# Performance work log

Measured on AMD Instinct MI355X. Metric: run time of the kernel, lower is better.

## Reference

```python
import jax, jax.numpy as jnp
import numpy as np

N_PATHS = 8
T2_EFF = 0.5 * 100.0 + 0.5 * (100 // 50)  # p_dimer*T2_dimer + p_trimer*T2_trimer = 51.0
J_FREQ = 20.0


def setup_inputs() -> dict:
    key = jax.random.key(0)
    ks = jax.random.split(key, 5)
    B, D, H, P = 2048, 1024, 1024, N_PATHS
    return {
        "x": jax.random.normal(ks[0], (B, D), dtype=jnp.float32),
        "W_input": jax.random.normal(ks[1], (D, H), dtype=jnp.float32) * 0.1,
        "W_paths": jax.random.normal(ks[2], (P, H, H), dtype=jnp.float32) * 0.1,
        "J_coupling": jax.random.normal(ks[3], (P, P), dtype=jnp.float32) * 0.01,
        "coherent_state": jax.random.normal(ks[4], (B, P, H), dtype=jnp.float32),
        "t": jnp.ones((1,), dtype=jnp.float32),  # time_since_formation buffer
    }


def reference(x, W_input, W_paths, J_coupling, coherent_state, t):
    # base activation: [B, H]
    base = x @ W_input
    # all per-path matmuls batched into one einsum: [B, P, H]
    path_act = jnp.einsum("bh,phk->bpk", base, W_paths)
    # coherence decay gate (scalar, broadcasts)
    alpha = jnp.clip(jnp.exp(-t[0] / T2_EFF), 0.0, 1.0)
    superposition = alpha * coherent_state + (1.0 - alpha) * path_act
    # interference matrix from symmetrized J-coupling
    J_sym = 0.5 * (J_coupling + J_coupling.T)
    phase = 2.0 * jnp.pi * J_FREQ * t[0] / 1000.0
    interference = jax.nn.softmax(jnp.cos(phase * J_sym), axis=1)  # [P, P]
    # double-loop mixing == small matmul over path dim
    interfered = jnp.einsum("ij,bjh->bih", interference, superposition) / N_PATHS
    interfered = interfered * alpha  # coherence_factor == alpha
    # no measurement (default path): mean over paths
    return jnp.mean(interfered, axis=1)  # [B, H]
```

## Files before the change

kernel.cpp:

```cpp
#include <hip/hip_runtime.h>
#include <cstdint>


typedef __attribute__((ext_vector_type(8))) __bf16 bf16x8;
typedef __attribute__((ext_vector_type(4))) float f32x4;
typedef unsigned short u16;

__device__ __forceinline__ u16 f32_to_bf16_rne(float f) {
  unsigned int u = __float_as_uint(f);
  u += 0x7fffu + ((u >> 16) & 1u);
  return (u16)(u >> 16);
}

__device__ __forceinline__ f32x4 nt_load4(const float* p) {
  return __builtin_nontemporal_load((const f32x4*)p);
}

__device__ __forceinline__ void wave_scalars(const float* __restrict__ J,
                                             const float* __restrict__ t,
                                             float* w_out, float* alpha_out) {
  const int lane = threadIdx.x & 63;
  float tv = t[0];
  float alpha = fminf(fmaxf(expf(-tv / 51.0f), 0.0f), 1.0f);
  float phase = 2.0f * 3.14159265358979323846f * 20.0f * tv / 1000.0f;
  int i = lane >> 3, j = lane & 7;
  float jsym = 0.5f * (J[i * 8 + j] + J[j * 8 + i]);
  float e = expf(cosf(phase * jsym));
  float rs = e;
  rs += __shfl_xor(rs, 1);
  rs += __shfl_xor(rs, 2);
  rs += __shfl_xor(rs, 4);
  float p = e / rs;
  float cs = p;
  cs += __shfl_xor(cs, 8);
  cs += __shfl_xor(cs, 16);
  cs += __shfl_xor(cs, 32);
  *w_out = alpha * (1.0f / 64.0f) * cs;
  *alpha_out = alpha;
}

__device__ __forceinline__ void convert16(const float* __restrict__ src,
                                          u16* __restrict__ dst, u16* ld,
                                          int tid) {
  f32x4 v[16];
#pragma unroll
  for (int row = 0; row < 16; row++) v[row] = nt_load4(src + row * 1024 + tid * 4);
#pragma unroll
  for (int row = 0; row < 16; row++) {
    ushort4 o;
    o.x = f32_to_bf16_rne(v[row][0]);
    o.y = f32_to_bf16_rne(v[row][1]);
    o.z = f32_to_bf16_rne(v[row][2]);
    o.w = f32_to_bf16_rne(v[row][3]);
    *(ushort4*)(ld + row * 1032 + tid * 4) = o;
  }
  __syncthreads();
#pragma unroll
  for (int s = 0; s < 8; s++) {
    int idx = s * 256 + tid;
    int lf = idx & 63, kt = idx >> 6;
    int row = lf & 15, colb = kt * 32 + ((lf >> 4) << 3);
    *(uint4*)(dst + (kt * 64 + lf) * 8) = *(const uint4*)(ld + row * 1032 + colb);
  }
}

__global__ __launch_bounds__(256, 4) void k_prep(
    const float* __restrict__ win, const float* __restrict__ wp,
    const float* __restrict__ J, const float* __restrict__ t,
    u16* __restrict__ winfrag, u16* __restrict__ wefrag) {
  __shared__ __align__(16) char smem[33024];
  const int blk = blockIdx.x;
  const int tid = threadIdx.x;
  const int lane = tid & 63;

  if (blk < 512) {
    float* lt = (float*)smem;
    float wv, alpha;
    wave_scalars(J, t, &wv, &alpha);
    float wLO[8];
#pragma unroll
    for (int p = 0; p < 8; p++)
      wLO[p] = __shfl(wv, (lane & 56) | p) * (1.0f - alpha);
    const int a0 = (blk & 31) * 32;
    const int b0 = (blk >> 5) * 64;
    f32x4 v[2][8];
#pragma unroll
    for (int s = 0; s < 2; s++) {
      const int item = s * 256 + tid;
      const int row = item >> 4, ch = item & 15;
      const float* base = wp + (size_t)(a0 + row) * 1024 + b0 + ch * 4;
#pragma unroll
      for (int j = 0; j < 8; j++) v[s][j] = nt_load4(base + (size_t)j * 1048576);
    }
#pragma unroll
    for (int s = 0; s < 2; s++) {
      const int item = s * 256 + tid;
      const int row = item >> 4, ch = item & 15;
      f32x4 acc = {0.f, 0.f, 0.f, 0.f};
#pragma unroll
      for (int j = 0; j < 8; j++) acc += wLO[j] * v[s][j];
      *(f32x4*)&lt[row * 68 + ch * 4] = acc;
    }
    __syncthreads();
    {
      const int lf = tid & 63, rtl = tid >> 6;
      const int rowh2 = rtl * 16 + (lf & 15);
      const int kh1 = (lf >> 4) << 3;
      __align__(16) u16 o[8];
#pragma unroll
      for (int i = 0; i < 8; i++)
        o[i] = f32_to_bf16_rne(lt[(kh1 + i) * 68 + rowh2]);
      const int rt = (b0 >> 4) + rtl, kt = a0 >> 5;
      *(uint4*)(wefrag + ((size_t)(rt * 32 + kt) * 64 + lf) * 8) = *(const uint4*)o;
    }
  } else {
    const int cid = blk - 512;
    convert16(win + (size_t)cid * 16384, winfrag + (size_t)cid * 16384,
              (u16*)smem, tid);
  }
}

__global__ __launch_bounds__(256, 4) void k_mid(
    const float* __restrict__ x, const u16* __restrict__ Af,
    const u16* __restrict__ Bf, u16* __restrict__ xfrag,
    u16* __restrict__ ofrag) {
  __shared__ __align__(16) char smem[33024];
  const int blk = blockIdx.x;
  const int tid = threadIdx.x;

  if (blk < 512) {
    u16* ct = (u16*)smem;
    const int wave = tid >> 6, lane = tid & 63;
    const int quad = lane >> 4, t16 = lane & 15;
    const int xcd = blk & 7, i = blk >> 3;
    const int m0 = (xcd + 8 * (i & 1)) * 64;
    const int n0 = (i >> 1) * 32;
    const u16* ap = Af + ((size_t)((m0 + wave * 16) >> 4) * 32) * 512 + lane * 8;
    const u16* bp = Bf + ((size_t)(n0 >> 4) * 32) * 512 + lane * 8;

    f32x4 acc[2] = {{0.f, 0.f, 0.f, 0.f}, {0.f, 0.f, 0.f, 0.f}};
    for (int kb = 0; kb < 32; kb += 4) {
      bf16x8 a[4], b0[4], b1[4];
#pragma unroll
      for (int u = 0; u < 4; u++) {
        a[u] = *(const bf16x8*)(ap + (kb + u) * 512);
        b0[u] = *(const bf16x8*)(bp + (kb + u) * 512);
        b1[u] = *(const bf16x8*)(bp + (32 + kb + u) * 512);
      }
#pragma unroll
      for (int u = 0; u < 4; u++) {
        acc[0] = __builtin_amdgcn_mfma_f32_16x16x32_bf16(a[u], b0[u], acc[0], 0, 0, 0);
        acc[1] = __builtin_amdgcn_mfma_f32_16x16x32_bf16(a[u], b1[u], acc[1], 0, 0, 0);
      }
    }
#pragma unroll
    for (int r = 0; r < 4; r++)
#pragma unroll
      for (int ni = 0; ni < 2; ni++)
        ct[(wave * 16 + quad * 4 + r) * 36 + ni * 16 + t16] =
            f32_to_bf16_rne(acc[ni][r]);
    __syncthreads();
    {
      int lf = tid & 63, rtl = tid >> 6;
      int rowl = rtl * 16 + (lf & 15);
      int colb = (lf >> 4) << 3;
      __align__(16) u16 o[8];
#pragma unroll
      for (int i2 = 0; i2 < 8; i2++) o[i2] = ct[rowl * 36 + colb + i2];
      *(uint4*)(ofrag +
                ((size_t)(((m0 >> 4) + rtl) * 32 + (n0 >> 5)) * 64 + lf) * 8) =
          *(const uint4*)o;
    }
  } else {
    const int cid = blk - 512;
    convert16(x + (size_t)cid * 16384, xfrag + (size_t)cid * 16384, (u16*)smem,
              tid);
  }
}

__global__ __launch_bounds__(512, 4) void k_main(
    const u16* __restrict__ Af, const u16* __restrict__ Bf,
    const float* __restrict__ coh, const float* __restrict__ J,
    const float* __restrict__ t, float* __restrict__ out) {
  __shared__ float cs_lds[64 * 68];
  const int tid = threadIdx.x;
  const int wave = tid >> 6, lane = tid & 63;
  const int xcd = blockIdx.x & 7, i = blockIdx.x >> 3;
  const int m0 = (xcd + 8 * (i >> 4)) * 64;
  const int n0 = (i & 15) * 64;
  const int quad = lane >> 4, t16 = lane & 15;
  const int wm = (wave >> 1) * 32, wn = (wave & 1) * 32;

  f32x4 acc[2][2];
  if (wave < 4) {
    const u16* ap = Af + ((size_t)((m0 + wm) >> 4) * 32) * 512 + lane * 8;
    const u16* bp = Bf + ((size_t)((n0 + wn) >> 4) * 32) * 512 + lane * 8;
#pragma unroll
    for (int mi = 0; mi < 2; mi++)
#pragma unroll
      for (int ni = 0; ni < 2; ni++) acc[mi][ni] = (f32x4){0.f, 0.f, 0.f, 0.f};
    for (int kb = 0; kb < 32; kb += 4) {
      bf16x8 a0[4], a1[4], b0[4], b1[4];
#pragma unroll
      for (int u = 0; u < 4; u++) {
        a0[u] = *(const bf16x8*)(ap + (kb + u) * 512);
        a1[u] = *(const bf16x8*)(ap + (32 + kb + u) * 512);
        b0[u] = *(const bf16x8*)(bp + (kb + u) * 512);
        b1[u] = *(const bf16x8*)(bp + (32 + kb + u) * 512);
      }
#pragma unroll
      for (int u = 0; u < 4; u++) {
        acc[0][0] = __builtin_amdgcn_mfma_f32_16x16x32_bf16(a0[u], b0[u], acc[0][0], 0, 0, 0);
        acc[0][1] = __builtin_amdgcn_mfma_f32_16x16x32_bf16(a0[u], b1[u], acc[0][1], 0, 0, 0);
        acc[1][0] = __builtin_amdgcn_mfma_f32_16x16x32_bf16(a1[u], b0[u], acc[1][0], 0, 0, 0);
        acc[1][1] = __builtin_amdgcn_mfma_f32_16x16x32_bf16(a1[u], b1[u], acc[1][1], 0, 0, 0);
      }
    }
  } else {
    float wv, alpha;
    wave_scalars(J, t, &wv, &alpha);
    float wHI[8];
#pragma unroll
    for (int p = 0; p < 8; p++) wHI[p] = __shfl(wv, (lane & 56) | p) * alpha;
    const int tc = (wave - 4) * 64 + lane;
    const int c4 = tc & 15;
    const int rb = tc >> 4;
    const float* cb = coh + (size_t)m0 * 8192 + n0 + c4 * 4;
#pragma unroll
    for (int up = 0; up < 2; up++) {
      f32x4 v[2][8];
#pragma unroll
      for (int h = 0; h < 2; h++) {
        const float* cr = cb + (size_t)(rb + 16 * (up * 2 + h)) * 8192;
#pragma unroll
        for (int p = 0; p < 8; p++) v[h][p] = nt_load4(cr + p * 1024);
      }
#pragma unroll
      for (int h = 0; h < 2; h++) {
        f32x4 a4 = {0.f, 0.f, 0.f, 0.f};
#pragma unroll
        for (int p = 0; p < 8; p++) a4 += wHI[p] * v[h][p];
        *(f32x4*)&cs_lds[(rb + 16 * (up * 2 + h)) * 68 + c4 * 4] = a4;
      }
    }
  }
  __syncthreads();
  if (wave < 4) {
#pragma unroll
    for (int mi = 0; mi < 2; mi++)
#pragma unroll
      for (int r = 0; r < 4; r++) {
        const int ml = wm + mi * 16 + quad * 4 + r;
        const size_t mrow = (size_t)(m0 + ml) * 1024;
#pragma unroll
        for (int ni = 0; ni < 2; ni++) {
          const int nl = wn + ni * 16 + t16;
          out[mrow + n0 + nl] = acc[mi][ni][r] + cs_lds[ml * 68 + nl];
        }
      }
  }
}

extern "C" void kernel_launch(void* const* d_in, const int* in_sizes, int n_in,
                              void* d_out, int out_size, void* d_ws, size_t ws_size,
                              hipStream_t stream) {
  const float* x   = (const float*)d_in[0];
  const float* win = (const float*)d_in[1];
  const float* wp  = (const float*)d_in[2];
  const float* J   = (const float*)d_in[3];
  const float* coh = (const float*)d_in[4];
  const float* t   = (const float*)d_in[5];
  float* out = (float*)d_out;

  char* ws = (char*)d_ws;
  u16* xfrag   = (u16*)ws;
  u16* winfrag = (u16*)(ws + 4u * 1024 * 1024);
  u16* wefrag  = (u16*)(ws + 6u * 1024 * 1024);
  u16* wctfrag = (u16*)(ws + 8u * 1024 * 1024);

  k_prep<<<576, 256, 0, stream>>>(win, wp, J, t, winfrag, wefrag);
  k_mid<<<640, 256, 0, stream>>>(x, wefrag, winfrag, xfrag, wctfrag);
  k_main<<<512, 512, 0, stream>>>(xfrag, wctfrag, coh, J, t, out);
}
```

Baseline: 157.1 us.

## Move x conversion into prep kernel and split main-kernel work across all waves

The x fp32-to-bf16 fragment conversion moves from the middle kernel into the prep kernel, so the middle kernel becomes a pure small GEMM. In the main kernel, all eight waves now first stream the coherent_state tile and reduce it into LDS, then all eight run the MFMA GEMM on smaller per-wave tiles. Each wave adds its accumulator into LDS, and the output is written with vectorized 16-byte stores. This replaces the earlier split where four waves did MFMA while four did the coherent-state load, at the cost of serializing the load phase before the GEMM and adding an extra barrier.

```diff
diff --git a/kernel.cpp b/kernel.cpp
--- a/kernel.cpp
+++ b/kernel.cpp
@@ -12,7 +12,7 @@
   return (u16)(u >> 16);
 }
 
-__device__ __forceinline__ f32x4 nt_load4(const float* p) {
+__device__ __forceinline__ f32x4 nt4(const float* p) {
   return __builtin_nontemporal_load((const f32x4*)p);
 }
 
@@ -44,7 +44,7 @@
                                           int tid) {
   f32x4 v[16];
 #pragma unroll
-  for (int row = 0; row < 16; row++) v[row] = nt_load4(src + row * 1024 + tid * 4);
+  for (int row = 0; row < 16; row++) v[row] = nt4(src + row * 1024 + tid * 4);
 #pragma unroll
   for (int row = 0; row < 16; row++) {
     ushort4 o;
@@ -65,8 +65,9 @@
 }
 
 __global__ __launch_bounds__(256, 4) void k_prep(
-    const float* __restrict__ win, const float* __restrict__ wp,
-    const float* __restrict__ J, const float* __restrict__ t,
+    const float* __restrict__ x, const float* __restrict__ win,
+    const float* __restrict__ wp, const float* __restrict__ J,
+    const float* __restrict__ t, u16* __restrict__ xfrag,
     u16* __restrict__ winfrag, u16* __restrict__ wefrag) {
   __shared__ __align__(16) char smem[33024];
   const int blk = blockIdx.x;
@@ -90,7 +91,7 @@
       const int row = item >> 4, ch = item & 15;
       const float* base = wp + (size_t)(a0 + row) * 1024 + b0 + ch * 4;
 #pragma unroll
-      for (int j = 0; j < 8; j++) v[s][j] = nt_load4(base + (size_t)j * 1048576);
+      for (int j = 0; j < 8; j++) v[s][j] = nt4(base + (size_t)j * 1048576);
     }
 #pragma unroll
     for (int s = 0; s < 2; s++) {
@@ -113,68 +114,62 @@
       const int rt = (b0 >> 4) + rtl, kt = a0 >> 5;
       *(uint4*)(wefrag + ((size_t)(rt * 32 + kt) * 64 + lf) * 8) = *(const uint4*)o;
     }
-  } else {
-    const int cid = blk - 512;
-    convert16(win + (size_t)cid * 16384, winfrag + (size_t)cid * 16384,
-              (u16*)smem, tid);
-  }
-}
-
-__global__ __launch_bounds__(256, 4) void k_mid(
-    const float* __restrict__ x, const u16* __restrict__ Af,
-    const u16* __restrict__ Bf, u16* __restrict__ xfrag,
-    u16* __restrict__ ofrag) {
-  __shared__ __align__(16) char smem[33024];
-  const int blk = blockIdx.x;
-  const int tid = threadIdx.x;
-
-  if (blk < 512) {
-    u16* ct = (u16*)smem;
-    const int wave = tid >> 6, lane = tid & 63;
-    const int quad = lane >> 4, t16 = lane & 15;
-    const int xcd = blk & 7, i = blk >> 3;
-    const int m0 = (xcd + 8 * (i & 1)) * 64;
-    const int n0 = (i >> 1) * 32;
-    const u16* ap = Af + ((size_t)((m0 + wave * 16) >> 4) * 32) * 512 + lane * 8;
-    const u16* bp = Bf + ((size_t)(n0 >> 4) * 32) * 512 + lane * 8;
-
-    f32x4 acc[2] = {{0.f, 0.f, 0.f, 0.f}, {0.f, 0.f, 0.f, 0.f}};
-    for (int kb = 0; kb < 32; kb += 4) {
-      bf16x8 a[4], b0[4], b1[4];
-#pragma unroll
-      for (int u = 0; u < 4; u++) {
-        a[u] = *(const bf16x8*)(ap + (kb + u) * 512);
-        b0[u] = *(const bf16x8*)(bp + (kb + u) * 512);
-        b1[u] = *(const bf16x8*)(bp + (32 + kb + u) * 512);
-      }
-#pragma unroll
-      for (int u = 0; u < 4; u++) {
-        acc[0] = __builtin_amdgcn_mfma_f32_16x16x32_bf16(a[u], b0[u], acc[0], 0, 0, 0);
-        acc[1] = __builtin_amdgcn_mfma_f32_16x16x32_bf16(a[u], b1[u], acc[1], 0, 0, 0);
-      }
-    }
-#pragma unroll
-    for (int r = 0; r < 4; r++)
-#pragma unroll
-      for (int ni = 0; ni < 2; ni++)
-        ct[(wave * 16 + quad * 4 + r) * 36 + ni * 16 + t16] =
-            f32_to_bf16_rne(acc[ni][r]);
-    __syncthreads();
-    {
-      int lf = tid & 63, rtl = tid >> 6;
-      int rowl = rtl * 16 + (lf & 15);
-      int colb = (lf >> 4) << 3;
-      __align__(16) u16 o[8];
-#pragma unroll
-      for (int i2 = 0; i2 < 8; i2++) o[i2] = ct[rowl * 36 + colb + i2];
-      *(uint4*)(ofrag +
-                ((size_t)(((m0 >> 4) + rtl) * 32 + (n0 >> 5)) * 64 + lf) * 8) =
-          *(const uint4*)o;
-    }
-  } else {
+  } else if (blk < 640) {
     const int cid = blk - 512;
     convert16(x + (size_t)cid * 16384, xfrag + (size_t)cid * 16384, (u16*)smem,
               tid);
+  } else {
+    const int cid = blk - 640;
+    convert16(win + (size_t)cid * 16384, winfrag + (size_t)cid * 16384,
+              (u16*)smem, tid);
+  }
+}
+
+__global__ __launch_bounds__(256, 4) void k_gemm0(const u16* __restrict__ Af,
+                                                  const u16* __restrict__ Bf,
+                                                  u16* __restrict__ ofrag) {
+  __shared__ u16 ct[64 * 36];
+  const int tid = threadIdx.x;
+  const int wave = tid >> 6, lane = tid & 63;
+  const int quad = lane >> 4, t16 = lane & 15;
+  const int xcd = blockIdx.x & 7, i = blockIdx.x >> 3;
+  const int m0 = (xcd + 8 * (i & 1)) * 64;
+  const int n0 = (i >> 1) * 32;
+  const u16* ap = Af + ((size_t)((m0 + wave * 16) >> 4) * 32) * 512 + lane * 8;
+  const u16* bp = Bf + ((size_t)(n0 >> 4) * 32) * 512 + lane * 8;
+
+  f32x4 acc[2] = {{0.f, 0.f, 0.f, 0.f}, {0.f, 0.f, 0.f, 0.f}};
+  for (int kb = 0; kb < 32; kb += 4) {
+    bf16x8 a[4], b0[4], b1[4];
+#pragma unroll
+    for (int u = 0; u < 4; u++) {
+      a[u] = *(const bf16x8*)(ap + (kb + u) * 512);
+      b0[u] = *(const bf16x8*)(bp + (kb + u) * 512);
+      b1[u] = *(const bf16x8*)(bp + (32 + kb + u) * 512);
+    }
+#pragma unroll
+    for (int u = 0; u < 4; u++) {
+      acc[0] = __builtin_amdgcn_mfma_f32_16x16x32_bf16(a[u], b0[u], acc[0], 0, 0, 0);
+      acc[1] = __builtin_amdgcn_mfma_f32_16x16x32_bf16(a[u], b1[u], acc[1], 0, 0, 0);
+    }
+  }
+#pragma unroll
+  for (int r = 0; r < 4; r++)
+#pragma unroll
+    for (int ni = 0; ni < 2; ni++)
+      ct[(wave * 16 + quad * 4 + r) * 36 + ni * 16 + t16] =
+          f32_to_bf16_rne(acc[ni][r]);
+  __syncthreads();
+  {
+    int lf = tid & 63, rtl = tid >> 6;
+    int rowl = rtl * 16 + (lf & 15);
+    int colb = (lf >> 4) << 3;
+    __align__(16) u16 o[8];
+#pragma unroll
+    for (int i2 = 0; i2 < 8; i2++) o[i2] = ct[rowl * 36 + colb + i2];
+    *(uint4*)(ofrag +
+              ((size_t)(((m0 >> 4) + rtl) * 32 + (n0 >> 5)) * 64 + lf) * 8) =
+        *(const uint4*)o;
   }
 }
 
@@ -182,82 +177,76 @@
     const u16* __restrict__ Af, const u16* __restrict__ Bf,
     const float* __restrict__ coh, const float* __restrict__ J,
     const float* __restrict__ t, float* __restrict__ out) {
-  __shared__ float cs_lds[64 * 68];
+  __shared__ float cs[64 * 68];
   const int tid = threadIdx.x;
   const int wave = tid >> 6, lane = tid & 63;
+  const int quad = lane >> 4, t16 = lane & 15;
   const int xcd = blockIdx.x & 7, i = blockIdx.x >> 3;
   const int m0 = (xcd + 8 * (i >> 4)) * 64;
   const int n0 = (i & 15) * 64;
-  const int quad = lane >> 4, t16 = lane & 15;
-  const int wm = (wave >> 1) * 32, wn = (wave & 1) * 32;
-
-  f32x4 acc[2][2];
-  if (wave < 4) {
+
+  float wv, alpha;
+  wave_scalars(J, t, &wv, &alpha);
+  float wHI[8];
+#pragma unroll
+  for (int p = 0; p < 8; p++) wHI[p] = __shfl(wv, (lane & 56) | p) * alpha;
+
+  {
+    f32x4 v[2][8];
+#pragma unroll
+    for (int c = 0; c < 2; c++) {
+      const int pair = c * 512 + tid;
+      const int row = pair >> 4, ch = pair & 15;
+      const float* cb = coh + (size_t)(m0 + row) * 8192 + n0 + ch * 4;
+#pragma unroll
+      for (int p = 0; p < 8; p++) v[c][p] = nt4(cb + p * 1024);
+    }
+#pragma unroll
+    for (int c = 0; c < 2; c++) {
+      const int pair = c * 512 + tid;
+      const int row = pair >> 4, ch = pair & 15;
+      f32x4 a = {0.f, 0.f, 0.f, 0.f};
+#pragma unroll
+      for (int p = 0; p < 8; p++) a += wHI[p] * v[c][p];
+      *(f32x4*)&cs[row * 68 + ch * 4] = a;
+    }
+  }
+  __syncthreads();
+
+  {
+    const int wm = (wave >> 2) * 32, wn = (wave & 3) * 16;
     const u16* ap = Af + ((size_t)((m0 + wm) >> 4) * 32) * 512 + lane * 8;
     const u16* bp = Bf + ((size_t)((n0 + wn) >> 4) * 32) * 512 + lane * 8;
-#pragma unroll
-    for (int mi = 0; mi < 2; mi++)
-#pragma unroll
-      for (int ni = 0; ni < 2; ni++) acc[mi][ni] = (f32x4){0.f, 0.f, 0.f, 0.f};
+    f32x4 acc[2] = {{0.f, 0.f, 0.f, 0.f}, {0.f, 0.f, 0.f, 0.f}};
     for (int kb = 0; kb < 32; kb += 4) {
-      bf16x8 a0[4], a1[4], b0[4], b1[4];
+      bf16x8 a0[4], a1[4], b[4];
 #pragma unroll
       for (int u = 0; u < 4; u++) {
         a0[u] = *(const bf16x8*)(ap + (kb + u) * 512);
         a1[u] = *(const bf16x8*)(ap + (32 + kb + u) * 512);
-        b0[u] = *(const bf16x8*)(bp + (kb + u) * 512);
-        b1[u] = *(const bf16x8*)(bp + (32 + kb + u) * 512);
+        b[u] = *(const bf16x8*)(bp + (kb + u) * 512);
       }
 #pragma unroll
       for (int u = 0; u < 4; u++) {
-        acc[0][0] = __builtin_amdgcn_mfma_f32_16x16x32_bf16(a0[u], b0[u], acc[0][0], 0, 0, 0);
-        acc[0][1] = __builtin_amdgcn_mfma_f32_16x16x32_bf16(a0[u], b1[u], acc[0][1], 0, 0, 0);
-        acc[1][0] = __builtin_amdgcn_mfma_f32_16x16x32_bf16(a1[u], b0[u], acc[1][0], 0, 0, 0);
-        acc[1][1] = __builtin_amdgcn_mfma_f32_16x16x32_bf16(a1[u], b1[u], acc[1][1], 0, 0, 0);
+        acc[0] = __builtin_amdgcn_mfma_f32_16x16x32_bf16(a0[u], b[u], acc[0], 0, 0, 0);
+        acc[1] = __builtin_amdgcn_mfma_f32_16x16x32_bf16(a1[u], b[u], acc[1], 0, 0, 0);
       }
     }
-  } else {
-    float wv, alpha;
-    wave_scalars(J, t, &wv, &alpha);
-    float wHI[8];
-#pragma unroll
-    for (int p = 0; p < 8; p++) wHI[p] = __shfl(wv, (lane & 56) | p) * alpha;
-    const int tc = (wave - 4) * 64 + lane;
-    const int c4 = tc & 15;
-    const int rb = tc >> 4;
-    const float* cb = coh + (size_t)m0 * 8192 + n0 + c4 * 4;
-#pragma unroll
-    for (int up = 0; up < 2; up++) {
-      f32x4 v[2][8];
-#pragma unroll
-      for (int h = 0; h < 2; h++) {
-        const float* cr = cb + (size_t)(rb + 16 * (up * 2 + h)) * 8192;
-#pragma unroll
-        for (int p = 0; p < 8; p++) v[h][p] = nt_load4(cr + p * 1024);
-      }
-#pragma unroll
-      for (int h = 0; h < 2; h++) {
-        f32x4 a4 = {0.f, 0.f, 0.f, 0.f};
-#pragma unroll
-        for (int p = 0; p < 8; p++) a4 += wHI[p] * v[h][p];
-        *(f32x4*)&cs_lds[(rb + 16 * (up * 2 + h)) * 68 + c4 * 4] = a4;
-      }
-    }
-  }
-  __syncthreads();
-  if (wave < 4) {
+    __syncthreads();
 #pragma unroll
     for (int mi = 0; mi < 2; mi++)
 #pragma unroll
-      for (int r = 0; r < 4; r++) {
-        const int ml = wm + mi * 16 + quad * 4 + r;
-        const size_t mrow = (size_t)(m0 + ml) * 1024;
-#pragma unroll
-        for (int ni = 0; ni < 2; ni++) {
-          const int nl = wn + ni * 16 + t16;
-          out[mrow + n0 + nl] = acc[mi][ni][r] + cs_lds[ml * 68 + nl];
-        }
-      }
+      for (int r = 0; r < 4; r++)
+        cs[(wm + mi * 16 + quad * 4 + r) * 68 + wn + t16] += acc[mi][r];
+  }
+  __syncthreads();
+
+#pragma unroll
+  for (int c = 0; c < 2; c++) {
+    const int pair = c * 512 + tid;
+    const int row = pair >> 4, ch = pair & 15;
+    *(f32x4*)(out + (size_t)(m0 + row) * 1024 + n0 + ch * 4) =
+        *(const f32x4*)&cs[row * 68 + ch * 4];
   }
 }
 
@@ -278,7 +267,7 @@
   u16* wefrag  = (u16*)(ws + 6u * 1024 * 1024);
   u16* wctfrag = (u16*)(ws + 8u * 1024 * 1024);
 
-  k_prep<<<576, 256, 0, stream>>>(win, wp, J, t, winfrag, wefrag);
-  k_mid<<<640, 256, 0, stream>>>(x, wefrag, winfrag, xfrag, wctfrag);
+  k_prep<<<704, 256, 0, stream>>>(x, win, wp, J, t, xfrag, winfrag, wefrag);
+  k_gemm0<<<512, 256, 0, stream>>>(wefrag, winfrag, wctfrag);
   k_main<<<512, 512, 0, stream>>>(xfrag, wctfrag, coh, J, t, out);
 }
```

Result: no change. 158.8 us (+1.1%).
